# Kernel optimization log

Hardware: AMD Instinct MI355X
Metric: run time of the kernel (lower is better)

The kernel has to match this reference:

```python
import jax, jax.numpy as jnp
import numpy as np

B, N1, N2, D, H = 2, 1024, 1024, 2048, 16
DH = D // H  # 128


def _rope_tables(S, d):
    inv = 1.0 / (10000.0 ** (np.arange(0, d, 2, dtype=np.float32) / d))
    ang = np.outer(np.arange(S, dtype=np.float32), inv)  # [S, d/2]
    cos = np.repeat(np.cos(ang), 2, axis=-1).astype(np.float32)  # [S, d] interleaved pairs
    sin = np.repeat(np.sin(ang), 2, axis=-1).astype(np.float32)
    return jnp.asarray(cos), jnp.asarray(sin)


def setup_inputs() -> dict:
    key = jax.random.key(0)
    ks = jax.random.split(key, 24)
    sc = 0.02
    cos1, sin1 = _rope_tables(N1, DH)
    cos2, sin2 = _rope_tables(N2, DH)
    inp = {
        'x_1': jax.random.normal(ks[0], (B, N1, D), dtype=jnp.float32),
        'x_2': jax.random.normal(ks[1], (B, N2, D), dtype=jnp.float32),
        'cos1': cos1, 'sin1': sin1, 'cos2': cos2, 'sin2': sin2,
    }
    names = ['wq1', 'wk1', 'wv1', 'wo1', 'wq2', 'wk2', 'wv2', 'wo2']
    for i, n in enumerate(names):
        inp[n] = jax.random.normal(ks[2 + i], (D, D), dtype=jnp.float32) * sc
        inp['b' + n[1:]] = jax.random.normal(ks[10 + i], (D,), dtype=jnp.float32) * sc
    return inp


def _apply_rope(x, cos, sin):
    # x: [B, H, S, DH]; interleaved-pair rotation (use_real_unbind_dim=-1)
    xr = x.reshape(*x.shape[:-1], -1, 2)
    x_real, x_imag = xr[..., 0], xr[..., 1]
    x_rot = jnp.stack([-x_imag, x_real], axis=-1).reshape(x.shape)
    return x * cos[None, None] + x_rot * sin[None, None]


def _split_heads(t):
    b, n, _ = t.shape
    return t.reshape(b, n, H, DH).transpose(0, 2, 1, 3)  # b h n c


def reference(x_1, x_2, cos1, sin1, cos2, sin2,
              wq1, bq1, wk1, bk1, wv1, bv1, wo1, bo1,
              wq2, bq2, wk2, bk2, wv2, bv2, wo2, bo2):
    len_1 = x_1.shape[1]
    q = jnp.concatenate([x_1 @ wq1 + bq1, x_2 @ wq2 + bq2], axis=1)
    k = jnp.concatenate([x_1 @ wk1 + bk1, x_2 @ wk2 + bk2], axis=1)
    v = jnp.concatenate([x_1 @ wv1 + bv1, x_2 @ wv2 + bv2], axis=1)
    q, k, v = _split_heads(q), _split_heads(k), _split_heads(v)
    q = q * (DH ** -0.5)
    # per-position RoPE on the concatenated stream == per-stream RoPE then concat
    cos = jnp.concatenate([cos1, cos2], axis=0)
    sin = jnp.concatenate([sin1, sin2], axis=0)
    q = _apply_rope(q, cos, sin)
    k = _apply_rope(k, cos, sin)
    # joint attention over both streams (independent/cross_only flags = False)
    scores = jnp.einsum('bhqd,bhkd->bhqk', q, k)
    attn = jax.nn.softmax(scores, axis=-1)
    o = jnp.einsum('bhqk,bhkd->bhqd', attn, v)
    o = o.transpose(0, 2, 1, 3).reshape(o.shape[0], -1, H * DH)  # b n (h c)
    o1 = o[:, :len_1] @ wo1 + bo1
    o2 = o[:, len_1:] @ wo2 + bo2
    return (o1, o2)
```

## Files before the change

### kernel.cpp

```cpp
#include <hip/hip_runtime.h>
#include <hip/hip_bf16.h>

typedef __attribute__((ext_vector_type(4))) float f32x4;
typedef __attribute__((ext_vector_type(8))) short short8;
typedef __attribute__((ext_vector_type(4))) unsigned short us4;
typedef __attribute__((ext_vector_type(2))) unsigned short us2;
typedef unsigned short u16;

__device__ __forceinline__ float bf2f(u16 u) {
  unsigned int x = ((unsigned int)u) << 16;
  float f; __builtin_memcpy(&f, &x, 4); return f;
}
__device__ __forceinline__ u16 f2bf(float f) {
  __hip_bfloat16 h = __float2bfloat16(f);
  u16 u; __builtin_memcpy(&u, &h, 2); return u;
}

#define GLL16(g, l) __builtin_amdgcn_global_load_lds( \
    (const __attribute__((address_space(1))) unsigned int*)(g), \
    (__attribute__((address_space(3))) unsigned int*)(l), 16, 0, 0)

#define MFMA16x32(a, b, c) __builtin_amdgcn_mfma_f32_16x16x32_bf16(a, b, c, 0, 0, 0)


__global__ __launch_bounds__(256) void k_convert_x(const float* __restrict__ x1,
                                                   const float* __restrict__ x2,
                                                   u16* __restrict__ xc) {
  int tid = blockIdx.x * 256 + threadIdx.x;
  int e = tid * 8;
  int m = e >> 11, d = e & 2047;
  int b = m >> 11, n = m & 2047;
  const float* src = (n < 1024) ? (x1 + ((b << 10) + n) * 2048 + d)
                                : (x2 + ((b << 10) + n - 1024) * 2048 + d);
  float4 v0 = *(const float4*)src;
  float4 v1 = *(const float4*)(src + 4);
  us4 a = {f2bf(v0.x), f2bf(v0.y), f2bf(v0.z), f2bf(v0.w)};
  us4 c = {f2bf(v1.x), f2bf(v1.y), f2bf(v1.z), f2bf(v1.w)};
  *(us4*)(xc + e) = a;
  *(us4*)(xc + e + 4) = c;
}

struct W8 { const float* w[8]; };

__global__ __launch_bounds__(256) void k_wt(W8 p, u16* __restrict__ wtbase) {
  __shared__ u16 lt[64][72];
  const float* W = p.w[blockIdx.z];
  u16* Wt = wtbase + (size_t)blockIdx.z * 4194304u;
  int k0 = blockIdx.x * 64, n0 = blockIdx.y * 64;
  int t = threadIdx.x;
#pragma unroll
  for (int i = 0; i < 4; ++i) {
    int lin = t + i * 256;
    int r = lin >> 4, c4 = (lin & 15) * 4;
    float4 v = *(const float4*)&W[(k0 + r) * 2048 + n0 + c4];
    us4 u = {f2bf(v.x), f2bf(v.y), f2bf(v.z), f2bf(v.w)};
    *(us4*)&lt[r][c4] = u;
  }
  __syncthreads();
#pragma unroll
  for (int i = 0; i < 8; ++i) {
    int lin = t + i * 256;
    int rd = lin >> 5, cs = (lin & 31) * 2;
    us2 u = {lt[cs][rd], lt[cs + 1][rd]};
    *(us2*)&Wt[(n0 + rd) * 2048 + k0 + cs] = u;
  }
}

__global__ __launch_bounds__(256) void k_vt(const u16* __restrict__ V, u16* __restrict__ Vt) {
  __shared__ u16 lt[64][72];
  int b = blockIdx.z;
  int s0 = blockIdx.x * 64, d0 = blockIdx.y * 64;
  int t = threadIdx.x;
#pragma unroll
  for (int i = 0; i < 2; ++i) {
    int lin = t + i * 256;
    int r = lin >> 3, c8 = (lin & 7) * 8;
    short8 v = *(const short8*)&V[(b * 2048 + s0 + r) * 2048 + d0 + c8];
    *(short8*)&lt[r][c8] = v;
  }
  __syncthreads();
#pragma unroll
  for (int i = 0; i < 8; ++i) {
    int lin = t + i * 256;
    int rd = lin >> 5, cs = (lin & 31) * 2;
    us2 u = {lt[cs][rd], lt[cs + 1][rd]};
    *(us2*)&Vt[(b * 2048 + d0 + rd) * 2048 + s0 + cs] = u;
  }
}

__global__ __launch_bounds__(256) void k_rope(u16* __restrict__ Qb, u16* __restrict__ Kb,
                                              const float* __restrict__ cos1,
                                              const float* __restrict__ sin1,
                                              const float* __restrict__ cos2,
                                              const float* __restrict__ sin2) {
  u16* T = blockIdx.y ? Kb : Qb;
  const float scale = blockIdx.y ? 1.f : 0.08838834764831843f;
  int tid = blockIdx.x * 256 + threadIdx.x;
  int e = tid * 8;
  int m = e >> 11;
  int n = m & 2047;
  int dh0 = e & 127;
  const float* cr; const float* sr;
  if (n < 1024) { cr = cos1 + n * 128; sr = sin1 + n * 128; }
  else          { cr = cos2 + (n - 1024) * 128; sr = sin2 + (n - 1024) * 128; }
  float4 c0 = *(const float4*)(cr + dh0), c1 = *(const float4*)(cr + dh0 + 4);
  float4 s0 = *(const float4*)(sr + dh0), s1 = *(const float4*)(sr + dh0 + 4);
  short8 xv = *(short8*)(T + e);
  float x0 = bf2f((u16)xv[0]), x1 = bf2f((u16)xv[1]), x2 = bf2f((u16)xv[2]), x3 = bf2f((u16)xv[3]);
  float x4 = bf2f((u16)xv[4]), x5 = bf2f((u16)xv[5]), x6 = bf2f((u16)xv[6]), x7 = bf2f((u16)xv[7]);
  us4 o0 = { f2bf((x0 * c0.x - x1 * s0.x) * scale), f2bf((x1 * c0.x + x0 * s0.x) * scale),
             f2bf((x2 * c0.z - x3 * s0.z) * scale), f2bf((x3 * c0.z + x2 * s0.z) * scale) };
  us4 o1 = { f2bf((x4 * c1.x - x5 * s1.x) * scale), f2bf((x5 * c1.x + x4 * s1.x) * scale),
             f2bf((x6 * c1.z - x7 * s1.z) * scale), f2bf((x7 * c1.z + x6 * s1.z) * scale) };
  *(us4*)(T + e) = o0;
  *(us4*)(T + e + 4) = o1;
}

__device__ __forceinline__ void gemm8_core(const u16* __restrict__ A,
                                           const u16* __restrict__ Bt,
                                           int m0, int nb,
                                           u16* lA, u16* lB,
                                           f32x4 acc[8][2]) {
  const int t = threadIdx.x;
  const int lane = t & 63, wid = t >> 6;
  const int lq = lane & 15, lg = lane >> 4;
  const int wr = wid >> 2, wc = wid & 3;
  const int swz = (lq & 7) << 4;

  u16* lA0 = lA;             u16* lA1 = lA + 256 * 64;
  u16* lB0 = lB;             u16* lB1 = lB + 128 * 64;

  short8 af[4][2], bf[2][2];

  auto stA = [&](u16* lbase, int kt, int half) {
    const int k0 = (kt & 31) * 64;
#pragma unroll
    for (int j = 0; j < 2; ++j) {
      int r = j * 128 + half * 64 + (t >> 3);
      int colb = (t & 7) * 16;
      int sc = colb ^ ((r & 7) << 4);
      GLL16(A + (size_t)(m0 + r) * 2048 + k0 + (sc >> 1),
            (u16*)((char*)lbase + r * 128 + colb));
    }
  };
  auto stB = [&](u16* lbase, int kt, int qn) {
    const int k0 = (kt & 31) * 64;
    int row = (t >> 7) * 32 + qn * 16 + ((t >> 3) & 15);
    int colb = (t & 7) * 16;
    int sc = colb ^ ((row & 7) << 4);
    GLL16(Bt + (size_t)(nb + row) * 2048 + k0 + (sc >> 1),
          (u16*)((char*)lbase + row * 128 + colb));
  };
  auto rdA = [&](const u16* lbase, int qm) {
#pragma unroll
    for (int mf = 0; mf < 4; ++mf)
#pragma unroll
      for (int kc = 0; kc < 2; ++kc) {
        int row = wr * 128 + (qm * 4 + mf) * 16 + lq;
        af[mf][kc] = *(const short8*)((const char*)lbase + row * 128 +
                                      ((kc * 64 + lg * 16) ^ swz));
      }
  };
  auto rdB = [&](const u16* lbase, int qn) {
#pragma unroll
    for (int kc = 0; kc < 2; ++kc) {
      int row = wc * 32 + qn * 16 + lq;
      bf[qn][kc] = *(const short8*)((const char*)lbase + row * 128 +
                                    ((kc * 64 + lg * 16) ^ swz));
    }
  };
  auto mm = [&](int qm, int qn) {
    __builtin_amdgcn_s_setprio(1);
#pragma unroll
    for (int mf = 0; mf < 4; ++mf)
#pragma unroll
      for (int kc = 0; kc < 2; ++kc)
        acc[qm * 4 + mf][qn] = MFMA16x32(af[mf][kc], bf[qn][kc], acc[qm * 4 + mf][qn]);
    __builtin_amdgcn_s_setprio(0);
    __builtin_amdgcn_sched_barrier(0);
  };

#define LGK0() do { asm volatile("s_waitcnt lgkmcnt(0)" ::: "memory"); \
                    __builtin_amdgcn_sched_barrier(0); } while (0)
#define BAR()  __builtin_amdgcn_s_barrier()
#define VM3()  asm volatile("s_waitcnt vmcnt(3)" ::: "memory")

  stA(lA0, 0, 0); stB(lB0, 0, 0); stA(lA0, 0, 1); stB(lB0, 0, 1);
  stA(lA1, 1, 0); stB(lB1, 1, 0);
  VM3();
  BAR();

#pragma unroll 1
  for (int i = 0; i < 16; ++i) {
    const int t1 = 2 * i + 1;
    rdA(lA0, 0); rdB(lB0, 0);
    stA(lA1, t1, 1);
    BAR(); LGK0(); mm(0, 0); BAR();
    rdB(lB0, 1);
    stB(lB1, t1, 1);
    BAR(); LGK0(); mm(0, 1); BAR();
    rdA(lA0, 1);
    stA(lA0, t1 + 1, 0);
    BAR(); LGK0(); mm(1, 0); BAR();
    stB(lB0, t1 + 1, 0);
    BAR(); LGK0(); mm(1, 1);
    VM3(); BAR();
    rdA(lA1, 0); rdB(lB1, 0);
    stA(lA0, t1 + 1, 1);
    BAR(); LGK0(); mm(0, 0); BAR();
    rdB(lB1, 1);
    stB(lB0, t1 + 1, 1);
    BAR(); LGK0(); mm(0, 1); BAR();
    rdA(lA1, 1);
    stA(lA1, t1 + 2, 0);
    BAR(); LGK0(); mm(1, 0); BAR();
    stB(lB1, t1 + 2, 0);
    BAR(); LGK0(); mm(1, 1);
    VM3(); BAR();
  }
#undef LGK0
#undef BAR
#undef VM3
}

struct QKV8P {
  const u16* wt[6];
  const float* bias[6];
  u16* out[3];
  const u16* xc;
};

__global__ __launch_bounds__(512, 2) void k_gemm_qkv(QKV8P p) {
  __shared__ __align__(16) u16 lA[2 * 256 * 64];
  __shared__ __align__(16) u16 lB[2 * 128 * 64];
  const int id = blockIdx.x;
  const int xcd = id & 7, wg = id >> 3;
  const int mt = wg & 15, nt = xcd * 6 + (wg >> 4);
  const int m0 = mt * 256;
  const int type = nt >> 4;
  const int colw = (nt & 15) * 128;
  const int strm = (mt >> 2) & 1;
  const int widx = type * 2 + strm;
  f32x4 acc[8][2];
  const f32x4 z4 = {0.f, 0.f, 0.f, 0.f};
#pragma unroll
  for (int a = 0; a < 8; ++a) { acc[a][0] = z4; acc[a][1] = z4; }
  gemm8_core(p.xc, p.wt[widx], m0, colw, lA, lB, acc);
  const int lane = threadIdx.x & 63, wid = threadIdx.x >> 6;
  const int lq = lane & 15, lg = lane >> 4;
  const int wr = wid >> 2, wc = wid & 3;
  u16* out = p.out[type];
  const float* bias = p.bias[widx];
#pragma unroll
  for (int nf = 0; nf < 2; ++nf) {
    int col = colw + wc * 32 + nf * 16 + lq;
    float bv = bias[col];
#pragma unroll
    for (int mf = 0; mf < 8; ++mf) {
      int row0 = m0 + wr * 128 + mf * 16 + lg * 4;
#pragma unroll
      for (int j = 0; j < 4; ++j)
        out[(size_t)(row0 + j) * 2048 + col] = f2bf(acc[mf][nf][j] + bv);
    }
  }
}

__global__ __launch_bounds__(512, 2) void k_gemm_out(const u16* __restrict__ O,
                                                     const u16* __restrict__ wt0,
                                                     const u16* __restrict__ wt1,
                                                     const float* __restrict__ b0,
                                                     const float* __restrict__ b1,
                                                     float* __restrict__ out) {
  __shared__ __align__(16) u16 lA[2 * 256 * 64];
  __shared__ __align__(16) u16 lB[2 * 128 * 64];
  const int id = blockIdx.x;
  const int xcd = id & 7, wg = id >> 3;
  const int mt = wg & 15, nt = xcd * 2 + (wg >> 4);
  const int m0 = mt * 256;
  const int strm = (mt >> 2) & 1;
  f32x4 acc[8][2];
  const f32x4 z4 = {0.f, 0.f, 0.f, 0.f};
#pragma unroll
  for (int a = 0; a < 8; ++a) { acc[a][0] = z4; acc[a][1] = z4; }
  gemm8_core(O, strm ? wt1 : wt0, m0, nt * 128, lA, lB, acc);
  const float* bias = strm ? b1 : b0;
  float* obase = strm ? out + 4194304 : out;
  const int lane = threadIdx.x & 63, wid = threadIdx.x >> 6;
  const int lq = lane & 15, lg = lane >> 4;
  const int wr = wid >> 2, wc = wid & 3;
#pragma unroll
  for (int nf = 0; nf < 2; ++nf) {
    int col = nt * 128 + wc * 32 + nf * 16 + lq;
    float bv = bias[col];
#pragma unroll
    for (int mf = 0; mf < 8; ++mf) {
      int row0 = m0 + wr * 128 + mf * 16 + lg * 4;
#pragma unroll
      for (int j = 0; j < 4; ++j) {
        int row = row0 + j;
        int b = row >> 11, n = row & 2047;
        obase[(size_t)(b * 1024 + n - strm * 1024) * 2048 + col] = acc[mf][nf][j] + bv;
      }
    }
  }
}

__global__ __launch_bounds__(256) void k_attn(const u16* __restrict__ Q,
                                              const u16* __restrict__ K,
                                              const u16* __restrict__ Vt,
                                              u16* __restrict__ O) {
  __shared__ __align__(16) u16 kbuf[2][64 * 128];
  __shared__ __align__(16) u16 vbuf[2][128 * 64];
  __shared__ __align__(16) u16 pbuf[4][16 * 88];
  const int t = threadIdx.x, lane = t & 63, w = t >> 6;
  const int lq = lane & 15, g = lane >> 4;
  const int id = blockIdx.x;
  const int lgid = (id & 7) * 64 + (id >> 3);
  const int bh = lgid >> 4, qt = lgid & 15;
  const int b = bh >> 4, h = bh & 15;

  short8 qf[2][4];
#pragma unroll
  for (int u = 0; u < 2; ++u) {
    const u16* Qp = Q + (size_t)(b * 2048 + qt * 128 + w * 32 + u * 16 + lq) * 2048
                    + h * 128 + g * 8;
#pragma unroll
    for (int c = 0; c < 4; ++c) qf[u][c] = *(const short8*)(Qp + c * 32);
  }

  f32x4 oacc[2][8];
  const f32x4 z4 = {0.f, 0.f, 0.f, 0.f};
#pragma unroll
  for (int u = 0; u < 2; ++u)
#pragma unroll
    for (int dc = 0; dc < 8; ++dc) oacc[u][dc] = z4;
  float m_run[2] = {-1e30f, -1e30f}, l_run[2] = {0.f, 0.f};

  const int swz = (lq & 7) << 4;

  auto STAGE = [&](int bs, int kt) {
#pragma unroll
    for (int ii = 0; ii < 4; ++ii) {
      int i = w * 4 + ii;
      int o = i * 1024 + lane * 16;
      {
        int row = o >> 8, colb = o & 255;
        int sc = colb ^ ((row & 7) << 4);
        GLL16(K + (size_t)(b * 2048 + kt + row) * 2048 + h * 128 + (sc >> 1),
              (u16*)((char*)kbuf[bs] + o));
      }
      {
        int row = o >> 7, colb = o & 127;
        int sc = colb ^ ((row & 7) << 4);
        GLL16(Vt + (size_t)(b * 2048 + h * 128 + row) * 2048 + kt + (sc >> 1),
              (u16*)((char*)vbuf[bs] + o));
      }
    }
  };

  STAGE(0, 0);
  asm volatile("s_waitcnt vmcnt(0)" ::: "memory");
  __syncthreads();

  for (int tt = 0; tt < 32; ++tt) {
    const int cb = tt & 1;
    if (tt < 31) STAGE(cb ^ 1, (tt + 1) * 64);

    const char* kb = (const char*)kbuf[cb];
    const char* vb = (const char*)vbuf[cb];
    f32x4 s[2][4];
#pragma unroll
    for (int u = 0; u < 2; ++u)
#pragma unroll
      for (int kg = 0; kg < 4; ++kg) s[u][kg] = z4;
#pragma unroll
    for (int c = 0; c < 4; ++c) {
#pragma unroll
      for (int kg = 0; kg < 4; ++kg) {
        short8 kf = *(const short8*)(kb + (kg * 16 + lq) * 256 + ((c * 64 + g * 16) ^ swz));
        s[0][kg] = MFMA16x32(kf, qf[0][c], s[0][kg]);
        s[1][kg] = MFMA16x32(kf, qf[1][c], s[1][kg]);
      }
    }
    u16* pw = pbuf[w];
    short8 pb[2][2];
#pragma unroll
    for (int u = 0; u < 2; ++u) {
      float pm = -1e30f;
#pragma unroll
      for (int kg = 0; kg < 4; ++kg)
#pragma unroll
        for (int j = 0; j < 4; ++j) pm = fmaxf(pm, s[u][kg][j]);
      pm = fmaxf(pm, __shfl_xor(pm, 16));
      pm = fmaxf(pm, __shfl_xor(pm, 32));
      const float mnew = fmaxf(m_run[u], pm);
      const float r = __expf(m_run[u] - mnew);
      m_run[u] = mnew;
      float ps = 0.f;
#pragma unroll
      for (int kg = 0; kg < 4; ++kg) {
        float p0 = __expf(s[u][kg][0] - mnew), p1 = __expf(s[u][kg][1] - mnew);
        float p2 = __expf(s[u][kg][2] - mnew), p3 = __expf(s[u][kg][3] - mnew);
        ps += (p0 + p1) + (p2 + p3);
        us4 wv = {f2bf(p0), f2bf(p1), f2bf(p2), f2bf(p3)};
        *(us4*)(pw + lq * 88 + kg * 16 + g * 4) = wv;
      }
      ps += __shfl_xor(ps, 16);
      ps += __shfl_xor(ps, 32);
      l_run[u] = l_run[u] * r + ps;
#pragma unroll
      for (int dc = 0; dc < 8; ++dc) oacc[u][dc] = oacc[u][dc] * r;
      pb[u][0] = *(const short8*)(pw + lq * 88 + g * 8);
      pb[u][1] = *(const short8*)(pw + lq * 88 + 32 + g * 8);
    }
#pragma unroll
    for (int kc = 0; kc < 2; ++kc) {
#pragma unroll
      for (int dc = 0; dc < 8; ++dc) {
        short8 vf = *(const short8*)(vb + (dc * 16 + lq) * 128 + ((kc * 64 + g * 16) ^ swz));
        oacc[0][dc] = MFMA16x32(vf, pb[0][kc], oacc[0][dc]);
        oacc[1][dc] = MFMA16x32(vf, pb[1][kc], oacc[1][dc]);
      }
    }
    asm volatile("s_waitcnt vmcnt(0)" ::: "memory");
    __syncthreads();
  }

#pragma unroll
  for (int u = 0; u < 2; ++u) {
    const float inv = 1.f / l_run[u];
    u16* Op = O + (size_t)(b * 2048 + qt * 128 + w * 32 + u * 16 + lq) * 2048
              + h * 128 + g * 4;
#pragma unroll
    for (int dc = 0; dc < 8; ++dc) {
      us4 ov = {f2bf(oacc[u][dc][0] * inv), f2bf(oacc[u][dc][1] * inv),
                f2bf(oacc[u][dc][2] * inv), f2bf(oacc[u][dc][3] * inv)};
      *(us4*)(Op + dc * 16) = ov;
    }
  }
}


extern "C" void kernel_launch(void* const* d_in, const int* in_sizes, int n_in,
                              void* d_out, int out_size, void* d_ws, size_t ws_size,
                              hipStream_t stream) {
  const float* x1   = (const float*)d_in[0];
  const float* x2   = (const float*)d_in[1];
  const float* cos1 = (const float*)d_in[2];
  const float* sin1 = (const float*)d_in[3];
  const float* cos2 = (const float*)d_in[4];
  const float* sin2 = (const float*)d_in[5];
  W8 wp; const float* bias[8];
  for (int i = 0; i < 8; ++i) {
    wp.w[i] = (const float*)d_in[6 + 2 * i];
    bias[i] = (const float*)d_in[7 + 2 * i];
  }
  float* out = (float*)d_out;
  u16* ws = (u16*)d_ws;
  const size_t NX = 8388608;
  const size_t WSZ = 4194304;
  u16* xc = ws;
  u16* wt = ws + NX;
  u16* Qb = wt + 8 * WSZ;
  u16* Kb = Qb + NX;
  u16* Vb = Kb + NX;
  u16* Ob = Vb + NX;
  u16* Vt = xc;
  if (ws_size < (size_t)((Ob + NX) - ws) * sizeof(u16)) return;

  k_convert_x<<<dim3(4096), dim3(256), 0, stream>>>(x1, x2, xc);
  k_wt<<<dim3(32, 32, 8), dim3(256), 0, stream>>>(wp, wt);

  QKV8P qp;
  qp.wt[0] = wt + 0 * WSZ; qp.wt[1] = wt + 4 * WSZ;
  qp.wt[2] = wt + 1 * WSZ; qp.wt[3] = wt + 5 * WSZ;
  qp.wt[4] = wt + 2 * WSZ; qp.wt[5] = wt + 6 * WSZ;
  qp.bias[0] = bias[0]; qp.bias[1] = bias[4];
  qp.bias[2] = bias[1]; qp.bias[3] = bias[5];
  qp.bias[4] = bias[2]; qp.bias[5] = bias[6];
  qp.out[0] = Qb; qp.out[1] = Kb; qp.out[2] = Vb;
  qp.xc = xc;
  k_gemm_qkv<<<dim3(768), dim3(512), 0, stream>>>(qp);

  k_rope<<<dim3(4096, 2), dim3(256), 0, stream>>>(Qb, Kb, cos1, sin1, cos2, sin2);
  k_vt<<<dim3(32, 32, 2), dim3(256), 0, stream>>>(Vb, Vt);
  k_attn<<<dim3(512), dim3(256), 0, stream>>>(Qb, Kb, Vt, Ob);
  k_gemm_out<<<dim3(256), dim3(512), 0, stream>>>(Ob, wt + 3 * WSZ, wt + 7 * WSZ,
                                                  bias[3], bias[7], out);
}
```

Before: 403.0 us.

## Enlarge GEMM tiles to 256x256 for QKV and output projections

Widens the block tile of the shared GEMM core from 256x128 to 256x256. Each wave now holds 128x64 accumulators, and B staging is unified with A staging. This raises arithmetic intensity per LDS and global load and halves the block count, at the cost of more registers and LDS (64KB per block). That may drop occupancy, and the out-projection grid of 128 blocks underfills the 256 CUs.

Result: faster. 387.9 us (-3.8%).

```diff
diff --git a/kernel.cpp b/kernel.cpp
--- a/kernel.cpp
+++ b/kernel.cpp
@@ -116,66 +116,65 @@
   *(us4*)(T + e + 4) = o1;
 }
 
-__device__ __forceinline__ void gemm8_core(const u16* __restrict__ A,
-                                           const u16* __restrict__ Bt,
-                                           int m0, int nb,
-                                           u16* lA, u16* lB,
-                                           f32x4 acc[8][2]) {
+__device__ __forceinline__ void gemm256_core(const u16* __restrict__ A,
+                                             const u16* __restrict__ Bt,
+                                             int m0, int nb,
+                                             u16* lA, u16* lB,
+                                             f32x4 acc[8][4]) {
   const int t = threadIdx.x;
   const int lane = t & 63, wid = t >> 6;
   const int lq = lane & 15, lg = lane >> 4;
   const int wr = wid >> 2, wc = wid & 3;
   const int swz = (lq & 7) << 4;
 
-  u16* lA0 = lA;             u16* lA1 = lA + 256 * 64;
-  u16* lB0 = lB;             u16* lB1 = lB + 128 * 64;
-
-  short8 af[4][2], bf[2][2];
-
-  auto stA = [&](u16* lbase, int kt, int half) {
+  u16* lA0 = lA;  u16* lA1 = lA + 256 * 64;
+  u16* lB0 = lB;  u16* lB1 = lB + 256 * 64;
+
+  short8 af[4][2];
+  short8 bf[2][2][2];
+
+  auto stage = [&](const u16* G, int grow0, u16* lbase, int h, int kt) {
     const int k0 = (kt & 31) * 64;
 #pragma unroll
     for (int j = 0; j < 2; ++j) {
-      int r = j * 128 + half * 64 + (t >> 3);
-      int colb = (t & 7) * 16;
-      int sc = colb ^ ((r & 7) << 4);
-      GLL16(A + (size_t)(m0 + r) * 2048 + k0 + (sc >> 1),
-            (u16*)((char*)lbase + r * 128 + colb));
+      int c = j * 512 + t;
+      int row = c >> 3;
+      int colb = (c & 7) * 16;
+      int sc = colb ^ ((row & 7) << 4);
+      GLL16(G + (size_t)(grow0 + h * 128 + row) * 2048 + k0 + (sc >> 1),
+            (u16*)((char*)lbase + (h * 128 + row) * 128 + colb));
     }
   };
-  auto stB = [&](u16* lbase, int kt, int qn) {
-    const int k0 = (kt & 31) * 64;
-    int row = (t >> 7) * 32 + qn * 16 + ((t >> 3) & 15);
-    int colb = (t & 7) * 16;
-    int sc = colb ^ ((row & 7) << 4);
-    GLL16(Bt + (size_t)(nb + row) * 2048 + k0 + (sc >> 1),
-          (u16*)((char*)lbase + row * 128 + colb));
-  };
-  auto rdA = [&](const u16* lbase, int qm) {
+  auto rdA = [&](const u16* lbase, int mh) {
 #pragma unroll
     for (int mf = 0; mf < 4; ++mf)
 #pragma unroll
       for (int kc = 0; kc < 2; ++kc) {
-        int row = wr * 128 + (qm * 4 + mf) * 16 + lq;
+        int row = wr * 128 + (mh * 4 + mf) * 16 + lq;
         af[mf][kc] = *(const short8*)((const char*)lbase + row * 128 +
                                       ((kc * 64 + lg * 16) ^ swz));
       }
   };
-  auto rdB = [&](const u16* lbase, int qn) {
-#pragma unroll
-    for (int kc = 0; kc < 2; ++kc) {
-      int row = wc * 32 + qn * 16 + lq;
-      bf[qn][kc] = *(const short8*)((const char*)lbase + row * 128 +
-                                    ((kc * 64 + lg * 16) ^ swz));
-    }
+  auto rdB = [&](const u16* lbase, int nh) {
+#pragma unroll
+    for (int nf = 0; nf < 2; ++nf)
+#pragma unroll
+      for (int kc = 0; kc < 2; ++kc) {
+        int row = wc * 64 + (nh * 2 + nf) * 16 + lq;
+        bf[nh][nf][kc] = *(const short8*)((const char*)lbase + row * 128 +
+                                          ((kc * 64 + lg * 16) ^ swz));
+      }
   };
-  auto mm = [&](int qm, int qn) {
+  auto mm = [&](int mh, int nh) {
     __builtin_amdgcn_s_setprio(1);
 #pragma unroll
     for (int mf = 0; mf < 4; ++mf)
 #pragma unroll
-      for (int kc = 0; kc < 2; ++kc)
-        acc[qm * 4 + mf][qn] = MFMA16x32(af[mf][kc], bf[qn][kc], acc[qm * 4 + mf][qn]);
+      for (int nf = 0; nf < 2; ++nf)
+#pragma unroll
+        for (int kc = 0; kc < 2; ++kc)
+          acc[mh * 4 + mf][nh * 2 + nf] =
+              MFMA16x32(af[mf][kc], bf[nh][nf][kc], acc[mh * 4 + mf][nh * 2 + nf]);
     __builtin_amdgcn_s_setprio(0);
     __builtin_amdgcn_sched_barrier(0);
   };
@@ -183,44 +182,48 @@
 #define LGK0() do { asm volatile("s_waitcnt lgkmcnt(0)" ::: "memory"); \
                     __builtin_amdgcn_sched_barrier(0); } while (0)
 #define BAR()  __builtin_amdgcn_s_barrier()
-#define VM3()  asm volatile("s_waitcnt vmcnt(3)" ::: "memory")
-
-  stA(lA0, 0, 0); stB(lB0, 0, 0); stA(lA0, 0, 1); stB(lB0, 0, 1);
-  stA(lA1, 1, 0); stB(lB1, 1, 0);
-  VM3();
+#define VM4()  asm volatile("s_waitcnt vmcnt(4)" ::: "memory")
+
+  stage(Bt, nb, lB0, 0, 0);
+  stage(A,  m0, lA0, 0, 0);
+  stage(Bt, nb, lB0, 1, 0);
+  stage(A,  m0, lA0, 1, 0);
+  stage(Bt, nb, lB1, 0, 1);
+  stage(A,  m0, lA1, 0, 1);
+  VM4();
   BAR();
 
 #pragma unroll 1
   for (int i = 0; i < 16; ++i) {
-    const int t1 = 2 * i + 1;
+    const int o1 = 2 * i + 1, e2 = 2 * i + 2, o3 = 2 * i + 3;
     rdA(lA0, 0); rdB(lB0, 0);
-    stA(lA1, t1, 1);
+    stage(Bt, nb, lB1, 1, o1);
     BAR(); LGK0(); mm(0, 0); BAR();
     rdB(lB0, 1);
-    stB(lB1, t1, 1);
+    stage(A, m0, lA1, 1, o1);
     BAR(); LGK0(); mm(0, 1); BAR();
     rdA(lA0, 1);
-    stA(lA0, t1 + 1, 0);
+    stage(Bt, nb, lB0, 0, e2);
     BAR(); LGK0(); mm(1, 0); BAR();
-    stB(lB0, t1 + 1, 0);
+    stage(A, m0, lA0, 0, e2);
     BAR(); LGK0(); mm(1, 1);
-    VM3(); BAR();
+    VM4(); BAR();
     rdA(lA1, 0); rdB(lB1, 0);
-    stA(lA0, t1 + 1, 1);
+    stage(Bt, nb, lB0, 1, e2);
     BAR(); LGK0(); mm(0, 0); BAR();
     rdB(lB1, 1);
-    stB(lB0, t1 + 1, 1);
+    stage(A, m0, lA0, 1, e2);
     BAR(); LGK0(); mm(0, 1); BAR();
     rdA(lA1, 1);
-    stA(lA1, t1 + 2, 0);
+    stage(Bt, nb, lB1, 0, o3);
     BAR(); LGK0(); mm(1, 0); BAR();
-    stB(lB1, t1 + 2, 0);
+    stage(A, m0, lA1, 0, o3);
     BAR(); LGK0(); mm(1, 1);
-    VM3(); BAR();
+    VM4(); BAR();
   }
 #undef LGK0
 #undef BAR
-#undef VM3
+#undef VM4
 }
 
 struct QKV8P {
@@ -232,28 +235,31 @@
 
 __global__ __launch_bounds__(512, 2) void k_gemm_qkv(QKV8P p) {
   __shared__ __align__(16) u16 lA[2 * 256 * 64];
-  __shared__ __align__(16) u16 lB[2 * 128 * 64];
+  __shared__ __align__(16) u16 lB[2 * 256 * 64];
   const int id = blockIdx.x;
-  const int xcd = id & 7, wg = id >> 3;
-  const int mt = wg & 15, nt = xcd * 6 + (wg >> 4);
+  const int xcd = id & 7, sub = id >> 3;
+  const int nt = xcd * 3 + (sub >> 4);
+  const int mt = sub & 15;
   const int m0 = mt * 256;
-  const int type = nt >> 4;
-  const int colw = (nt & 15) * 128;
+  const int type = nt >> 3;
+  const int colw = (nt & 7) * 256;
   const int strm = (mt >> 2) & 1;
   const int widx = type * 2 + strm;
-  f32x4 acc[8][2];
+  f32x4 acc[8][4];
   const f32x4 z4 = {0.f, 0.f, 0.f, 0.f};
 #pragma unroll
-  for (int a = 0; a < 8; ++a) { acc[a][0] = z4; acc[a][1] = z4; }
-  gemm8_core(p.xc, p.wt[widx], m0, colw, lA, lB, acc);
+  for (int a = 0; a < 8; ++a)
+#pragma unroll
+    for (int b = 0; b < 4; ++b) acc[a][b] = z4;
+  gemm256_core(p.xc, p.wt[widx], m0, colw, lA, lB, acc);
   const int lane = threadIdx.x & 63, wid = threadIdx.x >> 6;
   const int lq = lane & 15, lg = lane >> 4;
   const int wr = wid >> 2, wc = wid & 3;
   u16* out = p.out[type];
   const float* bias = p.bias[widx];
 #pragma unroll
-  for (int nf = 0; nf < 2; ++nf) {
-    int col = colw + wc * 32 + nf * 16 + lq;
+  for (int nf = 0; nf < 4; ++nf) {
+    int col = colw + wc * 64 + nf * 16 + lq;
     float bv = bias[col];
 #pragma unroll
     for (int mf = 0; mf < 8; ++mf) {
@@ -272,25 +278,26 @@
                                                      const float* __restrict__ b1,
                                                      float* __restrict__ out) {
   __shared__ __align__(16) u16 lA[2 * 256 * 64];
-  __shared__ __align__(16) u16 lB[2 * 128 * 64];
+  __shared__ __align__(16) u16 lB[2 * 256 * 64];
   const int id = blockIdx.x;
-  const int xcd = id & 7, wg = id >> 3;
-  const int mt = wg & 15, nt = xcd * 2 + (wg >> 4);
+  const int nt = id & 7, mt = id >> 3;
   const int m0 = mt * 256;
   const int strm = (mt >> 2) & 1;
-  f32x4 acc[8][2];
+  f32x4 acc[8][4];
   const f32x4 z4 = {0.f, 0.f, 0.f, 0.f};
 #pragma unroll
-  for (int a = 0; a < 8; ++a) { acc[a][0] = z4; acc[a][1] = z4; }
-  gemm8_core(O, strm ? wt1 : wt0, m0, nt * 128, lA, lB, acc);
+  for (int a = 0; a < 8; ++a)
+#pragma unroll
+    for (int b = 0; b < 4; ++b) acc[a][b] = z4;
+  gemm256_core(O, strm ? wt1 : wt0, m0, nt * 256, lA, lB, acc);
   const float* bias = strm ? b1 : b0;
   float* obase = strm ? out + 4194304 : out;
   const int lane = threadIdx.x & 63, wid = threadIdx.x >> 6;
   const int lq = lane & 15, lg = lane >> 4;
   const int wr = wid >> 2, wc = wid & 3;
 #pragma unroll
-  for (int nf = 0; nf < 2; ++nf) {
-    int col = nt * 128 + wc * 32 + nf * 16 + lq;
+  for (int nf = 0; nf < 4; ++nf) {
+    int col = nt * 256 + wc * 64 + nf * 16 + lq;
     float bv = bias[col];
 #pragma unroll
     for (int mf = 0; mf < 8; ++mf) {
@@ -480,11 +487,11 @@
   qp.bias[4] = bias[2]; qp.bias[5] = bias[6];
   qp.out[0] = Qb; qp.out[1] = Kb; qp.out[2] = Vb;
   qp.xc = xc;
-  k_gemm_qkv<<<dim3(768), dim3(512), 0, stream>>>(qp);
+  k_gemm_qkv<<<dim3(384), dim3(512), 0, stream>>>(qp);
 
   k_rope<<<dim3(4096, 2), dim3(256), 0, stream>>>(Qb, Kb, cos1, sin1, cos2, sin2);
   k_vt<<<dim3(32, 32, 2), dim3(256), 0, stream>>>(Vb, Vt);
   k_attn<<<dim3(512), dim3(256), 0, stream>>>(Qb, Kb, Vt, Ob);
-  k_gemm_out<<<dim3(256), dim3(512), 0, stream>>>(Ob, wt + 3 * WSZ, wt + 7 * WSZ,
+  k_gemm_out<<<dim3(128), dim3(512), 0, stream>>>(Ob, wt + 3 * WSZ, wt + 7 * WSZ,
                                                   bias[3], bias[7], out);
 }
```
